# Kernel tuning notes

Measured on AMD Instinct MI355X. Metric: run time of the kernel, lower is better.

The kernel has to match this reference:

```python
import jax, jax.numpy as jnp
import numpy as np

N = 2_000_000   # number of inversion targets
H = 64          # hidden width, arch = [1, H, H, 1]
MONO = 1e-3     # monotonic_const
N_ITER = 20     # bisection depth


def _apply_layers(x, pre_w1, b1, pre_w2, b2, pre_w3, b3):
    # PositiveLinear(A_constraint='exp') + Sigmoid stack; final layer also exp+sigmoid.
    h = jax.nn.sigmoid(x @ jnp.exp(pre_w1).T + b1)   # [N, H]
    h = jax.nn.sigmoid(h @ jnp.exp(pre_w2).T + b2)   # [N, H]
    y = jax.nn.sigmoid(h @ jnp.exp(pre_w3).T + b3)   # [N, 1]
    # d == 1, non_conditional_dim == 0 -> x[:, 0:1] == x
    return y + MONO * x


def setup_inputs() -> dict:
    key = jax.random.key(0)
    ks = jax.random.split(key, 7)

    def u(k, shape, lo, hi):
        return jax.random.uniform(k, shape, dtype=jnp.float32) * (hi - lo) + lo

    # exp-constraint init: pre_weight ~ U[log(0.01), log(sqrt(1/in_features))]
    lo1, hi1 = np.log(0.01), np.log(np.sqrt(1.0 / 1.0))
    loH, hiH = np.log(0.01), np.log(np.sqrt(1.0 / H))
    pre_w1 = u(ks[0], (H, 1), lo1, hi1)
    b1 = u(ks[1], (H,), -1.0, 1.0)            # scale = 1/in_features = 1
    pre_w2 = u(ks[2], (H, H), loH, hiH)
    b2 = u(ks[3], (H,), -1.0 / H, 1.0 / H)
    pre_w3 = u(ks[4], (1, H), loH, hiH)
    b3 = u(ks[5], (1,), -1.0 / H, 1.0 / H)
    z = jax.random.uniform(ks[6], (N, 1), dtype=jnp.float32)  # CDF targets in (0,1)
    return dict(z=z, pre_w1=pre_w1, b1=b1, pre_w2=pre_w2, b2=b2,
                pre_w3=pre_w3, b3=b3)


def reference(z, pre_w1, b1, pre_w2, b2, pre_w3, b3):
    A = lambda x: _apply_layers(x, pre_w1, b1, pre_w2, b2, pre_w3, b3)
    # scale(): F(x) = (A(x) - A(start)) / (A(end) - A(start)); d==1 so start=0, end=1
    a0 = A(jnp.zeros((1, 1), jnp.float32))
    a1 = A(jnp.ones((1, 1), jnp.float32))
    F = lambda q: (A(q) - a0) / (a1 - a0)

    # bisection_search: 20 interval halvings, return final midpoint (elementwise,
    # vectorized over the per-sample loop in the original F_inv)
    def body(_, carry):
        lo, hi = carry
        mid = (lo + hi) * 0.5
        gt = F(mid) > z
        return (jnp.where(gt, lo, mid), jnp.where(gt, mid, hi))

    lo, hi = jax.lax.fori_loop(0, N_ITER, body,
                               (jnp.zeros_like(z), jnp.ones_like(z)))
    return (lo + hi) * 0.5
```

## Files before the change

kernel.cpp:

```cpp
#include <hip/hip_runtime.h>


#define MONO 1e-3f
#define TLOG2 13
#define TSZ (1 << TLOG2)

typedef float fvec64 __attribute__((ext_vector_type(64)));

__device__ __forceinline__ float fast_rcp(float x) {
#if __has_builtin(__builtin_amdgcn_rcpf)
    return __builtin_amdgcn_rcpf(x);
#else
    return 1.0f / x;
#endif
}

__device__ __forceinline__ float sigmoidf_(float t) {
    return fast_rcp(1.0f + __expf(-t));
}

__global__ __launch_bounds__(256, 4) void fused_build_kernel(
        const float* __restrict__ pw1,
        const float* __restrict__ b1,
        const float* __restrict__ pw2,
        const float* __restrict__ b2,
        const float* __restrict__ pw3,
        const float* __restrict__ b3,
        float* __restrict__ T) {
    __shared__ __align__(16) float W2s[4096];
    __shared__ float part[256];

    int tid  = threadIdx.x;
#pragma unroll
    for (int i = 0; i < 16; ++i) {
        int idx = tid + i * 256;
        W2s[idx] = __expf(pw2[idx]);
    }
    __syncthreads();

    int lane = tid & 63;
    int sub = __builtin_amdgcn_readfirstlane(tid >> 6);
    int j = blockIdx.x * 64 + lane;
    int jc = j <= TSZ ? j : TSZ;
    float x = (float)jc * (1.0f / (float)TSZ);

    fvec64 h1;
#pragma unroll
    for (int k = 0; k < 64; ++k)
        h1[k] = sigmoidf_(fmaf(x, __expf(pw1[k]), b1[k]));

    float acc3 = 0.0f;
#pragma unroll
    for (int r = 0; r < 16; ++r) {
        int row = sub * 16 + r;
        float acc = b2[row];
        const float4* __restrict__ w4 =
            reinterpret_cast<const float4*>(&W2s[row * 64]);
#pragma unroll
        for (int q = 0; q < 16; ++q) {
            float4 w = w4[q];
            acc = fmaf(w.x, h1[4 * q + 0], acc);
            acc = fmaf(w.y, h1[4 * q + 1], acc);
            acc = fmaf(w.z, h1[4 * q + 2], acc);
            acc = fmaf(w.w, h1[4 * q + 3], acc);
        }
        acc3 = fmaf(__expf(pw3[row]), sigmoidf_(acc), acc3);
    }

    part[sub * 64 + lane] = acc3;
    __syncthreads();
    if (tid < 64 && j <= TSZ) {
        float s = part[lane] + part[64 + lane] + part[128 + lane]
                + part[192 + lane] + b3[0];
        T[j] = sigmoidf_(s) + MONO * x;
    }
}

__device__ __forceinline__ float search_one(float zv, const float* Ts,
                                            float a0, float scale) {
    float zt = fmaf(zv, scale, a0);
    int lo = 0;
#pragma unroll
    for (int s = TSZ >> 1; s >= 1; s >>= 1) {
        int c = lo + s;
        lo = (Ts[c] <= zt) ? c : lo;
    }
    float tl = Ts[lo];
    float th = Ts[lo + 1];
    float d = th - tl;
    float t = (d > 1e-30f) ? (zt - tl) * fast_rcp(d) : 0.5f;
    t = fminf(fmaxf(t, 0.0f), 1.0f);
    return ((float)lo + t) * (1.0f / (float)TSZ);
}

#define APPLY_BLOCKS 512

__global__ __launch_bounds__(256) void fused_apply_kernel(
        const float* __restrict__ z,
        const float* __restrict__ T,
        float* __restrict__ out, int n) {
    __shared__ __align__(16) float Ts[TSZ + 1];
    int tid = threadIdx.x;
#pragma unroll
    for (int i = 0; i < (TSZ / 4) / 256; ++i) {
        int idx = tid + i * 256;
        reinterpret_cast<float4*>(Ts)[idx] =
            reinterpret_cast<const float4*>(T)[idx];
    }
    if (tid == 0) Ts[TSZ] = T[TSZ];
    __syncthreads();

    float a0 = Ts[0];
    float scale = Ts[TSZ] - a0;

    int nv = n >> 2;
    int stride = gridDim.x * 256;
    for (int idx = blockIdx.x * 256 + tid; idx < nv; idx += stride) {
        float4 zz = reinterpret_cast<const float4*>(z)[idx];
        float4 oo;
        oo.x = search_one(zz.x, Ts, a0, scale);
        oo.y = search_one(zz.y, Ts, a0, scale);
        oo.z = search_one(zz.z, Ts, a0, scale);
        oo.w = search_one(zz.w, Ts, a0, scale);
        reinterpret_cast<float4*>(out)[idx] = oo;
    }
    int base = nv * 4;
    for (int t = base + blockIdx.x * 256 + tid; t < n; t += stride)
        out[t] = search_one(z[t], Ts, a0, scale);
}

extern "C" void kernel_launch(void* const* d_in, const int* in_sizes, int n_in,
                              void* d_out, int out_size, void* d_ws, size_t ws_size,
                              hipStream_t stream) {
    const float* z   = (const float*)d_in[0];
    const float* pw1 = (const float*)d_in[1];
    const float* b1  = (const float*)d_in[2];
    const float* pw2 = (const float*)d_in[3];
    const float* b2  = (const float*)d_in[4];
    const float* pw3 = (const float*)d_in[5];
    const float* b3  = (const float*)d_in[6];
    float* out = (float*)d_out;
    float* T   = (float*)d_ws;
    int n = in_sizes[0];

    fused_build_kernel<<<(TSZ + 1 + 63) / 64, 256, 0, stream>>>(
        pw1, b1, pw2, b2, pw3, b3, T);
    fused_apply_kernel<<<APPLY_BLOCKS, 256, 0, stream>>>(z, T, out, n);
}
```

Baseline: 99.87 us.

## Replace full binary search with bucketed index lookup table for table inversion

```diff
diff --git a/kernel.cpp b/kernel.cpp
--- a/kernel.cpp
+++ b/kernel.cpp
@@ -4,6 +4,9 @@
 #define MONO 1e-3f
 #define TLOG2 13
 #define TSZ (1 << TLOG2)
+#define BLOG2 13
+#define BSZ (1 << BLOG2)
+#define IDXN 8200
 
 typedef float fvec64 __attribute__((ext_vector_type(64)));
 
@@ -76,30 +79,56 @@
     }
 }
 
-__device__ __forceinline__ float search_one(float zv, const float* Ts,
-                                            float a0, float scale) {
-    float zt = fmaf(zv, scale, a0);
+__global__ __launch_bounds__(256) void build_idx_kernel(
+        const float* __restrict__ T,
+        unsigned short* __restrict__ IDX) {
+    int k = blockIdx.x * blockDim.x + threadIdx.x;
+    if (k > BSZ) return;
+    float a0 = T[0];
+    float a1 = T[TSZ];
+    float zb = fmaf((float)k * (1.0f / (float)BSZ), a1 - a0, a0);
     int lo = 0;
 #pragma unroll
     for (int s = TSZ >> 1; s >= 1; s >>= 1) {
         int c = lo + s;
-        lo = (Ts[c] <= zt) ? c : lo;
+        if (T[c] <= zb) lo = c;
+    }
+    if (T[TSZ] <= zb) lo = TSZ;
+    IDX[k] = (unsigned short)lo;
+}
+
+__device__ __forceinline__ float search_one(float zv, const float* Ts,
+                                            const unsigned short* IDXs,
+                                            float a0, float scale, float bscale) {
+    float zt = fmaf(zv, scale, a0);
+    int k = (int)((zt - a0) * bscale);
+    k = k < 0 ? 0 : (k > BSZ - 1 ? BSZ - 1 : k);
+    int lo = IDXs[k];
+    int hi = IDXs[k + 1];
+    if (hi > TSZ - 1) hi = TSZ - 1;
+    while (hi > lo) {
+        int mid = (lo + hi + 1) >> 1;
+        if (Ts[mid] <= zt) lo = mid; else hi = mid - 1;
     }
     float tl = Ts[lo];
     float th = Ts[lo + 1];
+    while (tl > zt && lo > 0)          { --lo; th = tl; tl = Ts[lo]; }
+    while (th <= zt && lo < TSZ - 1)   { ++lo; tl = th; th = Ts[lo + 1]; }
     float d = th - tl;
     float t = (d > 1e-30f) ? (zt - tl) * fast_rcp(d) : 0.5f;
     t = fminf(fmaxf(t, 0.0f), 1.0f);
     return ((float)lo + t) * (1.0f / (float)TSZ);
 }
 
-#define APPLY_BLOCKS 512
+#define APPLY_BLOCKS 768
 
-__global__ __launch_bounds__(256) void fused_apply_kernel(
+__global__ __launch_bounds__(256) void bucket_apply_kernel(
         const float* __restrict__ z,
         const float* __restrict__ T,
+        const unsigned short* __restrict__ IDX,
         float* __restrict__ out, int n) {
     __shared__ __align__(16) float Ts[TSZ + 1];
+    __shared__ __align__(16) unsigned short IDXs[IDXN];
     int tid = threadIdx.x;
 #pragma unroll
     for (int i = 0; i < (TSZ / 4) / 256; ++i) {
@@ -107,26 +136,31 @@
         reinterpret_cast<float4*>(Ts)[idx] =
             reinterpret_cast<const float4*>(T)[idx];
     }
+    for (int idx = tid; idx < IDXN / 8; idx += 256) {
+        reinterpret_cast<uint4*>(IDXs)[idx] =
+            reinterpret_cast<const uint4*>(IDX)[idx];
+    }
     if (tid == 0) Ts[TSZ] = T[TSZ];
     __syncthreads();
 
     float a0 = Ts[0];
     float scale = Ts[TSZ] - a0;
+    float bscale = (float)BSZ * fast_rcp(scale);
 
     int nv = n >> 2;
     int stride = gridDim.x * 256;
     for (int idx = blockIdx.x * 256 + tid; idx < nv; idx += stride) {
         float4 zz = reinterpret_cast<const float4*>(z)[idx];
         float4 oo;
-        oo.x = search_one(zz.x, Ts, a0, scale);
-        oo.y = search_one(zz.y, Ts, a0, scale);
-        oo.z = search_one(zz.z, Ts, a0, scale);
-        oo.w = search_one(zz.w, Ts, a0, scale);
+        oo.x = search_one(zz.x, Ts, IDXs, a0, scale, bscale);
+        oo.y = search_one(zz.y, Ts, IDXs, a0, scale, bscale);
+        oo.z = search_one(zz.z, Ts, IDXs, a0, scale, bscale);
+        oo.w = search_one(zz.w, Ts, IDXs, a0, scale, bscale);
         reinterpret_cast<float4*>(out)[idx] = oo;
     }
     int base = nv * 4;
     for (int t = base + blockIdx.x * 256 + tid; t < n; t += stride)
-        out[t] = search_one(z[t], Ts, a0, scale);
+        out[t] = search_one(z[t], Ts, IDXs, a0, scale, bscale);
 }
 
 extern "C" void kernel_launch(void* const* d_in, const int* in_sizes, int n_in,
@@ -141,9 +175,11 @@
     const float* b3  = (const float*)d_in[6];
     float* out = (float*)d_out;
     float* T   = (float*)d_ws;
+    unsigned short* IDX = (unsigned short*)((float*)d_ws + (TSZ + 1));
     int n = in_sizes[0];
 
     fused_build_kernel<<<(TSZ + 1 + 63) / 64, 256, 0, stream>>>(
         pw1, b1, pw2, b2, pw3, b3, T);
-    fused_apply_kernel<<<APPLY_BLOCKS, 256, 0, stream>>>(z, T, out, n);
+    build_idx_kernel<<<(BSZ + 1 + 255) / 256, 256, 0, stream>>>(T, IDX);
+    bucket_apply_kernel<<<APPLY_BLOCKS, 256, 0, stream>>>(z, T, IDX, out, n);
 }
```

Result: faster. 89.89 us (-10.0%).
